# Kernel tuning notes

Hardware: AMD Instinct MI355X
Metric: run time of the kernel (lower is better)

The kernel has to match this reference:

```python
import jax, jax.numpy as jnp
import numpy as np

N = 50000   # nodes
E = 800000  # edges
IN, HID, OUT, H = 128, 256, 128, 4
C1 = HID // H  # per-head channels for conv1/conv2
EPS_LN = 1e-5


def layer_norm(x, g, b):
    mu = x.mean(-1, keepdims=True)
    var = ((x - mu) ** 2).mean(-1, keepdims=True)
    return (x - mu) * jax.lax.rsqrt(var + EPS_LN) * g + b


def gatv2(x, src, dst, edge_attr, Wl, bl, Wr, br, We, att, bias, heads, ch, n):
    # PyG GATv2Conv (concat=True, negative_slope=0.2, share_weights=False)
    xl = (x @ Wl + bl).reshape(-1, heads, ch)   # [N,H,C] source transform
    xr = (x @ Wr + br).reshape(-1, heads, ch)   # [N,H,C] target transform
    e = (edge_attr @ We).reshape(-1, heads, ch) # [E,H,C] edge transform (no bias)
    m = jax.nn.leaky_relu(xl[src] + xr[dst] + e, 0.2)     # [E,H,C]
    logits = jnp.einsum('ehc,hc->eh', m, att)             # [E,H]
    mx = jax.ops.segment_max(logits, dst, num_segments=n) # segment softmax over dst
    a = jnp.exp(logits - mx[dst])
    denom = jax.ops.segment_sum(a, dst, num_segments=n)
    alpha = a / (denom[dst] + 1e-16)                      # [E,H]
    out = jax.ops.segment_sum(xl[src] * alpha[..., None], dst, num_segments=n)
    return out.reshape(-1, heads * ch) + bias


def setup_inputs() -> dict:
    key = jax.random.key(0)
    ks = jax.random.split(key, 24)
    s = 0.05
    inp = {
        'x': jax.random.normal(ks[0], (N, IN), jnp.float32),
        'edge_index': jax.random.randint(ks[1], (2, E), 0, N, jnp.int32),
        'edge_attr': jax.random.uniform(ks[2], (E, 1), jnp.float32),
        # conv1: in=IN, out per head=C1, heads=H
        'Wl1': jax.random.normal(ks[3], (IN, HID)) * s,  'bl1': jnp.zeros((HID,)),
        'Wr1': jax.random.normal(ks[4], (IN, HID)) * s,  'br1': jnp.zeros((HID,)),
        'We1': jax.random.normal(ks[5], (1, HID)) * s,
        'att1': jax.random.normal(ks[6], (H, C1)) * s,   'bo1': jnp.zeros((HID,)),
        'g1': jnp.ones((HID,)), 'be1': jnp.zeros((HID,)),
        # conv2: in=HID
        'Wl2': jax.random.normal(ks[7], (HID, HID)) * s, 'bl2': jnp.zeros((HID,)),
        'Wr2': jax.random.normal(ks[8], (HID, HID)) * s, 'br2': jnp.zeros((HID,)),
        'We2': jax.random.normal(ks[9], (1, HID)) * s,
        'att2': jax.random.normal(ks[10], (H, C1)) * s,  'bo2': jnp.zeros((HID,)),
        'g2': jnp.ones((HID,)), 'be2': jnp.zeros((HID,)),
        # conv3: heads=1, out=OUT
        'Wl3': jax.random.normal(ks[11], (HID, OUT)) * s, 'bl3': jnp.zeros((OUT,)),
        'Wr3': jax.random.normal(ks[12], (HID, OUT)) * s, 'br3': jnp.zeros((OUT,)),
        'We3': jax.random.normal(ks[13], (1, OUT)) * s,
        'att3': jax.random.normal(ks[14], (1, OUT)) * s,  'bo3': jnp.zeros((OUT,)),
        'g3': jnp.ones((OUT,)), 'be3': jnp.zeros((OUT,)),
    }
    return inp


def reference(x, edge_index, edge_attr,
              Wl1, bl1, Wr1, br1, We1, att1, bo1, g1, be1,
              Wl2, bl2, Wr2, br2, We2, att2, bo2, g2, be2,
              Wl3, bl3, Wr3, br3, We3, att3, bo3, g3, be3):
    src, dst = edge_index[0], edge_index[1]
    h = gatv2(x, src, dst, edge_attr, Wl1, bl1, Wr1, br1, We1, att1, bo1, H, C1, N)
    h = jax.nn.elu(layer_norm(h, g1, be1))  # dropout inactive at inference
    h = gatv2(h, src, dst, edge_attr, Wl2, bl2, Wr2, br2, We2, att2, bo2, H, C1, N)
    h = jax.nn.elu(layer_norm(h, g2, be2))
    h = gatv2(h, src, dst, edge_attr, Wl3, bl3, Wr3, br3, We3, att3, bo3, 1, OUT, N)
    return layer_norm(h, g3, be3)
```

## Files before the change

kernel.cpp:

```cpp
#include <hip/hip_runtime.h>
#include <cstdint>
#include <cstddef>

typedef unsigned short u16;
typedef __attribute__((ext_vector_type(8))) short short8v;
typedef __attribute__((ext_vector_type(4))) float f32x4;

#define IN_DIM 128
#define HID_DIM 256
#define OUT_DIM 128
#define HEADS 4

__device__ __forceinline__ float b2f(u16 v) {
    return __uint_as_float(((unsigned)v) << 16);
}
__device__ __forceinline__ u16 f2b(float f) {
    unsigned u = __float_as_uint(f);
    u += 0x7fffu + ((u >> 16) & 1u);
    return (u16)(u >> 16);
}


__global__ void count_k(const int* __restrict__ dst, int* __restrict__ counts, int ne) {
    int i = blockIdx.x * blockDim.x + threadIdx.x;
    if (i < ne) atomicAdd(&counts[dst[i]], 1);
}

__global__ __launch_bounds__(1024) void scan_k(const int* __restrict__ counts,
                                               int* __restrict__ offs,
                                               int* __restrict__ cursor, int n) {
    __shared__ int wtot[16];
    __shared__ int carry_s;
    int tid = threadIdx.x, wv = tid >> 6, ln = tid & 63;
    if (tid == 0) carry_s = 0;
    __syncthreads();
    for (int base = 0; base < n; base += 4096) {
        int i0 = base + tid * 4;
        int4 c4 = {0, 0, 0, 0};
        if (i0 + 3 < n) c4 = *(const int4*)(counts + i0);
        else {
            if (i0     < n) c4.x = counts[i0];
            if (i0 + 1 < n) c4.y = counts[i0 + 1];
            if (i0 + 2 < n) c4.z = counts[i0 + 2];
            if (i0 + 3 < n) c4.w = counts[i0 + 3];
        }
        int s0 = c4.x, s1 = s0 + c4.y, s2 = s1 + c4.z, s3 = s2 + c4.w;
        int v = s3;
#pragma unroll
        for (int o = 1; o < 64; o <<= 1) {
            int t = __shfl_up(v, o);
            if (ln >= o) v += t;
        }
        if (ln == 63) wtot[wv] = v;
        int wpref = v - s3;
        __syncthreads();
        if (wv == 0) {
            int w2 = (ln < 16) ? wtot[ln] : 0;
#pragma unroll
            for (int o = 1; o < 16; o <<= 1) {
                int t = __shfl_up(w2, o);
                if (ln >= o) w2 += t;
            }
            if (ln < 16) wtot[ln] = w2;
        }
        __syncthreads();
        int wbase = carry_s + (wv ? wtot[wv - 1] : 0);
        int ex0 = wbase + wpref;
        if (i0     < n) { offs[i0]     = ex0;      cursor[i0]     = ex0; }
        if (i0 + 1 < n) { offs[i0 + 1] = ex0 + s0; cursor[i0 + 1] = ex0 + s0; }
        if (i0 + 2 < n) { offs[i0 + 2] = ex0 + s1; cursor[i0 + 2] = ex0 + s1; }
        if (i0 + 3 < n) { offs[i0 + 3] = ex0 + s2; cursor[i0 + 3] = ex0 + s2; }
        __syncthreads();
        if (tid == 0) carry_s += wtot[15];
        __syncthreads();
    }
    if (threadIdx.x == 0) offs[n] = carry_s;
}

__global__ void fill_k(const int* __restrict__ src, const int* __restrict__ dst,
                       const float* __restrict__ ea, int* __restrict__ cursor,
                       int* __restrict__ csrc, float* __restrict__ cea, int ne) {
    int i = blockIdx.x * blockDim.x + threadIdx.x;
    if (i < ne) {
        int p = atomicAdd(&cursor[dst[i]], 1);
        csrc[p] = src[i];
        cea[p] = ea[i];
    }
}


template <int KG>
__global__ void xpack_k(const float* __restrict__ X, short* __restrict__ Xp, int total) {
    int gid = blockIdx.x * blockDim.x + threadIdx.x;
    if (gid >= total) return;
    int lane = gid & 63;
    int kg = (gid >> 6) % KG;
    int rt = gid / (64 * KG);
    int row = rt * 16 + (lane & 15);
    int k0 = kg * 32 + ((lane >> 4) << 3);
    const float* src = X + (size_t)row * (KG * 32) + k0;
    short8v o;
#pragma unroll
    for (int j = 0; j < 8; j++) o[j] = (short)f2b(src[j]);
    ((short8v*)Xp)[gid] = o;
}

template <int K, int HOUT>
__global__ void packw_k(const float* __restrict__ Wl, const float* __restrict__ Wr,
                        short* __restrict__ Wp) {
    constexpr int KG = K / 32;
    int gid = blockIdx.x * blockDim.x + threadIdx.x;
    int lane = gid & 63;
    int kg = (gid >> 6) % KG;
    int nt = gid / (64 * KG);
    int col = nt * 16 + (lane & 15);
    int k0 = kg * 32 + ((lane >> 4) << 3);
    const float* Wsrc = (col < HOUT) ? Wl : Wr;
    int c2 = (col < HOUT) ? col : col - HOUT;
    short8v o;
#pragma unroll
    for (int j = 0; j < 8; j++) o[j] = (short)f2b(Wsrc[(size_t)(k0 + j) * HOUT + c2]);
    ((short8v*)Wp)[gid] = o;
}


template <int KG, int NT, int HOUT, int R>
__global__ __launch_bounds__(256) void gemm_mfma(
    const short* __restrict__ Xp, const short* __restrict__ Wp,
    const float* __restrict__ bl, const float* __restrict__ br,
    u16* __restrict__ XL, u16* __restrict__ XR, int nrt) {
    constexpr int NCG = NT / 8;
    int w = threadIdx.x >> 6, lane = threadIdx.x & 63;
    int cg = blockIdx.x % NCG;
    int rt0 = (blockIdx.x / NCG) * R;
    if (rt0 >= nrt) return;
    int rcnt = min(R, nrt - rt0);
    int nt0 = cg * 8 + w * 2;
    const short8v* wb = (const short8v*)Wp + lane;
    short8v wf0[KG], wf1[KG];
#pragma unroll
    for (int kg = 0; kg < KG; kg++) {
        wf0[kg] = wb[(size_t)(nt0 * KG + kg) * 64];
        wf1[kg] = wb[(size_t)((nt0 + 1) * KG + kg) * 64];
    }
    int colg0 = nt0 * 16 + ((lane >> 4) << 2);
    int colg1 = colg0 + 16;
    bool isr0 = colg0 >= HOUT;
    bool isr1 = colg1 >= HOUT;
    int cl0 = colg0 - (isr0 ? HOUT : 0);
    int cl1 = colg1 - (isr1 ? HOUT : 0);
    float4 bb0 = *(const float4*)((isr0 ? br : bl) + cl0);
    float4 bb1 = *(const float4*)((isr1 ? br : bl) + cl1);
    u16* ob0 = (isr0 ? XR : XL) + cl0;
    u16* ob1 = (isr1 ? XR : XL) + cl1;

    const short8v* xb = (const short8v*)Xp + (size_t)rt0 * KG * 64 + lane;
    for (int r = 0; r < rcnt; ++r) {
        f32x4 acc0 = {0.f, 0.f, 0.f, 0.f}, acc1 = {0.f, 0.f, 0.f, 0.f};
#pragma unroll
        for (int kg = 0; kg < KG; kg++) {
            short8v xf = xb[(size_t)(r * KG + kg) * 64];
            acc0 = __builtin_amdgcn_mfma_f32_16x16x32_bf16(wf0[kg], xf, acc0, 0, 0, 0);
            acc1 = __builtin_amdgcn_mfma_f32_16x16x32_bf16(wf1[kg], xf, acc1, 0, 0, 0);
        }
        size_t rowoff = (size_t)((rt0 + r) * 16 + (lane & 15)) * HOUT;
        ushort4 o0 = { f2b(acc0[0] + bb0.x), f2b(acc0[1] + bb0.y),
                       f2b(acc0[2] + bb0.z), f2b(acc0[3] + bb0.w) };
        *(ushort4*)(ob0 + rowoff) = o0;
        ushort4 o1 = { f2b(acc1[0] + bb1.x), f2b(acc1[1] + bb1.y),
                       f2b(acc1[2] + bb1.z), f2b(acc1[3] + bb1.w) };
        *(ushort4*)(ob1 + rowoff) = o1;
    }
}


__global__ __launch_bounds__(256) void gat_fused4(
    const int* __restrict__ offs, const int* __restrict__ csrc, const float* __restrict__ cea,
    const float* __restrict__ We, const float* __restrict__ att,
    const u16* __restrict__ XL, const u16* __restrict__ XR,
    const float* __restrict__ bo, const float* __restrict__ g, const float* __restrict__ be,
    u16* __restrict__ hp, int n) {
    __shared__ int   sS[4][64];
    __shared__ float sEA[4][64];
    int tid = threadIdx.x;
    int w = tid >> 6;
    int lane = tid & 63;
    int node = blockIdx.x * 4 + w;
    int es = lane >> 5;
    int ls = lane & 31;
    int cabs = ls * 8;
    float xr[8], wev[8], atv[8];
    {
        short8v x8 = *(const short8v*)(XR + (size_t)node * 256 + cabs);
        float4 wA = *(const float4*)(We + cabs), wB = *(const float4*)(We + cabs + 4);
        float4 aA = *(const float4*)(att + cabs), aB = *(const float4*)(att + cabs + 4);
#pragma unroll
        for (int i = 0; i < 8; i++) xr[i] = b2f((u16)x8[i]);
        wev[0] = wA.x; wev[1] = wA.y; wev[2] = wA.z; wev[3] = wA.w;
        wev[4] = wB.x; wev[5] = wB.y; wev[6] = wB.z; wev[7] = wB.w;
        atv[0] = aA.x; atv[1] = aA.y; atv[2] = aA.z; atv[3] = aA.w;
        atv[4] = aB.x; atv[5] = aB.y; atv[6] = aB.z; atv[7] = aB.w;
    }
    int b0 = offs[node], eEnd = offs[node + 1];
    float dsum = 0.f;
    float acc[8];
#pragma unroll
    for (int i = 0; i < 8; i++) acc[i] = 0.f;
    for (int base = b0; base < eEnd; base += 64) {
        int cnt = min(64, eEnd - base);
        if (lane < cnt) { sS[w][lane] = csrc[base + lane]; sEA[w][lane] = cea[base + lane]; }
        short8v r0, r1, r2;
        float e0, e1f, e2;
        bool v0, v1, v2;
        {
            int j0 = es, j1 = es + 2, j2 = es + 4;
            v0 = j0 < cnt; v1 = j1 < cnt; v2 = j2 < cnt;
            int i0 = v0 ? j0 : 0, i1 = v1 ? j1 : 0, i2 = v2 ? j2 : 0;
            e0 = sEA[w][i0]; r0 = *(const short8v*)(XL + (size_t)sS[w][i0] * 256 + cabs);
            e1f = sEA[w][i1]; r1 = *(const short8v*)(XL + (size_t)sS[w][i1] * 256 + cabs);
            e2 = sEA[w][i2]; r2 = *(const short8v*)(XL + (size_t)sS[w][i2] * 256 + cabs);
        }
        for (int r = 0; r < cnt; r += 2) {
            short8v rc = r0; float ec = e0; bool vc = v0;
            r0 = r1; e0 = e1f; v0 = v1;
            r1 = r2; e1f = e2; v1 = v2;
            int jn = r + 6 + es;
            v2 = jn < cnt;
            int idx = v2 ? jn : 0;
            e2 = sEA[w][idx];
            r2 = *(const short8v*)(XL + (size_t)sS[w][idx] * 256 + cabs);
            float x[8];
#pragma unroll
            for (int i = 0; i < 8; i++) x[i] = b2f((u16)rc[i]);
            float p = 0.f;
#pragma unroll
            for (int i = 0; i < 8; i++) {
                float t = fmaf(ec, wev[i], x[i]) + xr[i];
                t = fmaxf(t, 0.2f * t);
                p += t * atv[i];
            }
            p += __shfl_xor(p, 1);
            p += __shfl_xor(p, 2);
            p += __shfl_xor(p, 4);
            float wv2 = vc ? __expf(p) : 0.f;
            dsum += wv2;
#pragma unroll
            for (int i = 0; i < 8; i++) acc[i] += wv2 * x[i];
        }
    }
    dsum += __shfl_xor(dsum, 32);
#pragma unroll
    for (int i = 0; i < 8; i++) acc[i] += __shfl_xor(acc[i], 32);
    float inv = 1.f / (dsum + 1e-16f);
    float4 bA = *(const float4*)(bo + cabs), bB = *(const float4*)(bo + cabs + 4);
    float v[8];
    v[0] = acc[0] * inv + bA.x; v[1] = acc[1] * inv + bA.y;
    v[2] = acc[2] * inv + bA.z; v[3] = acc[3] * inv + bA.w;
    v[4] = acc[4] * inv + bB.x; v[5] = acc[5] * inv + bB.y;
    v[6] = acc[6] * inv + bB.z; v[7] = acc[7] * inv + bB.w;
    float s1 = 0.f, s2 = 0.f;
#pragma unroll
    for (int i = 0; i < 8; i++) { s1 += v[i]; s2 += v[i] * v[i]; }
#pragma unroll
    for (int o = 16; o >= 1; o >>= 1) {
        s1 += __shfl_xor(s1, o);
        s2 += __shfl_xor(s2, o);
    }
    float mu = s1 / 256.f;
    float sinv = rsqrtf(s2 / 256.f - mu * mu + 1e-5f);
    if (es == 0) {
        float4 gA = *(const float4*)(g + cabs), gB = *(const float4*)(g + cabs + 4);
        float4 eA = *(const float4*)(be + cabs), eB = *(const float4*)(be + cabs + 4);
        float gg[8] = {gA.x, gA.y, gA.z, gA.w, gB.x, gB.y, gB.z, gB.w};
        float ee[8] = {eA.x, eA.y, eA.z, eA.w, eB.x, eB.y, eB.z, eB.w};
        short8v yv;
#pragma unroll
        for (int i = 0; i < 8; i++) {
            float y = (v[i] - mu) * sinv * gg[i] + ee[i];
            y = (y > 0.f) ? y : expm1f(y);
            yv[i] = (short)f2b(y);
        }
        int kg = cabs >> 5;
        int l = (node & 15) | (((cabs >> 3) & 3) << 4);
        size_t eoff = (((size_t)(node >> 4) * 8 + kg) * 64 + l) * 8;
        *(short8v*)(hp + eoff) = yv;
    }
}


__global__ __launch_bounds__(256) void gat_fused1(
    const int* __restrict__ offs, const int* __restrict__ csrc, const float* __restrict__ cea,
    const float* __restrict__ We, const float* __restrict__ att,
    const u16* __restrict__ XL, const u16* __restrict__ XR,
    const float* __restrict__ bo, const float* __restrict__ g, const float* __restrict__ be,
    float* __restrict__ out, int n) {
    __shared__ int   sS[4][64];
    __shared__ float sEA[4][64];
    int tid = threadIdx.x;
    int w = tid >> 6;
    int lane = tid & 63;
    int node = blockIdx.x * 4 + w;
    int q = lane >> 4;
    int ls = lane & 15;
    int cb = ls * 8;
    float xr[8], wev[8], atv[8];
    {
        short8v x8 = *(const short8v*)(XR + (size_t)node * 128 + cb);
        float4 wA = *(const float4*)(We + cb), wB = *(const float4*)(We + cb + 4);
        float4 aA = *(const float4*)(att + cb), aB = *(const float4*)(att + cb + 4);
#pragma unroll
        for (int i = 0; i < 8; i++) xr[i] = b2f((u16)x8[i]);
        wev[0] = wA.x; wev[1] = wA.y; wev[2] = wA.z; wev[3] = wA.w;
        wev[4] = wB.x; wev[5] = wB.y; wev[6] = wB.z; wev[7] = wB.w;
        atv[0] = aA.x; atv[1] = aA.y; atv[2] = aA.z; atv[3] = aA.w;
        atv[4] = aB.x; atv[5] = aB.y; atv[6] = aB.z; atv[7] = aB.w;
    }
    int b0 = offs[node], eEnd = offs[node + 1];
    float dsum = 0.f;
    float acc[8];
#pragma unroll
    for (int i = 0; i < 8; i++) acc[i] = 0.f;
    for (int base = b0; base < eEnd; base += 64) {
        int cnt = min(64, eEnd - base);
        if (lane < cnt) { sS[w][lane] = csrc[base + lane]; sEA[w][lane] = cea[base + lane]; }
        short8v r0, r1, r2;
        float e0, e1f, e2;
        bool v0, v1, v2;
        {
            int j0 = q, j1 = q + 4, j2 = q + 8;
            v0 = j0 < cnt; v1 = j1 < cnt; v2 = j2 < cnt;
            int i0 = v0 ? j0 : 0, i1 = v1 ? j1 : 0, i2 = v2 ? j2 : 0;
            e0 = sEA[w][i0]; r0 = *(const short8v*)(XL + (size_t)sS[w][i0] * 128 + cb);
            e1f = sEA[w][i1]; r1 = *(const short8v*)(XL + (size_t)sS[w][i1] * 128 + cb);
            e2 = sEA[w][i2]; r2 = *(const short8v*)(XL + (size_t)sS[w][i2] * 128 + cb);
        }
        for (int r = 0; r < cnt; r += 4) {
            short8v rc = r0; float ec = e0; bool vc = v0;
            r0 = r1; e0 = e1f; v0 = v1;
            r1 = r2; e1f = e2; v1 = v2;
            int jn = r + 12 + q;
            v2 = jn < cnt;
            int idx = v2 ? jn : 0;
            e2 = sEA[w][idx];
            r2 = *(const short8v*)(XL + (size_t)sS[w][idx] * 128 + cb);
            float x[8];
#pragma unroll
            for (int i = 0; i < 8; i++) x[i] = b2f((u16)rc[i]);
            float p = 0.f;
#pragma unroll
            for (int i = 0; i < 8; i++) {
                float t = fmaf(ec, wev[i], x[i]) + xr[i];
                t = fmaxf(t, 0.2f * t);
                p += t * atv[i];
            }
            p += __shfl_xor(p, 1);
            p += __shfl_xor(p, 2);
            p += __shfl_xor(p, 4);
            p += __shfl_xor(p, 8);
            float wv2 = vc ? __expf(p) : 0.f;
            dsum += wv2;
#pragma unroll
            for (int i = 0; i < 8; i++) acc[i] += wv2 * x[i];
        }
    }
    dsum += __shfl_xor(dsum, 32);
    dsum += __shfl_xor(dsum, 16);
#pragma unroll
    for (int i = 0; i < 8; i++) {
        acc[i] += __shfl_xor(acc[i], 32);
        acc[i] += __shfl_xor(acc[i], 16);
    }
    float inv = 1.f / (dsum + 1e-16f);
    float4 bA = *(const float4*)(bo + cb), bB = *(const float4*)(bo + cb + 4);
    float v[8];
    v[0] = acc[0] * inv + bA.x; v[1] = acc[1] * inv + bA.y;
    v[2] = acc[2] * inv + bA.z; v[3] = acc[3] * inv + bA.w;
    v[4] = acc[4] * inv + bB.x; v[5] = acc[5] * inv + bB.y;
    v[6] = acc[6] * inv + bB.z; v[7] = acc[7] * inv + bB.w;
    float s1 = 0.f, s2 = 0.f;
#pragma unroll
    for (int i = 0; i < 8; i++) { s1 += v[i]; s2 += v[i] * v[i]; }
#pragma unroll
    for (int o = 8; o >= 1; o >>= 1) {
        s1 += __shfl_xor(s1, o);
        s2 += __shfl_xor(s2, o);
    }
    float mu = s1 / 128.f;
    float sinv = rsqrtf(s2 / 128.f - mu * mu + 1e-5f);
    if (q == 0) {
        float4 gA = *(const float4*)(g + cb), gB = *(const float4*)(g + cb + 4);
        float4 eA = *(const float4*)(be + cb), eB = *(const float4*)(be + cb + 4);
        float gg[8] = {gA.x, gA.y, gA.z, gA.w, gB.x, gB.y, gB.z, gB.w};
        float ee[8] = {eA.x, eA.y, eA.z, eA.w, eB.x, eB.y, eB.z, eB.w};
        float4 oA, oB;
        oA.x = (v[0] - mu) * sinv * gg[0] + ee[0];
        oA.y = (v[1] - mu) * sinv * gg[1] + ee[1];
        oA.z = (v[2] - mu) * sinv * gg[2] + ee[2];
        oA.w = (v[3] - mu) * sinv * gg[3] + ee[3];
        oB.x = (v[4] - mu) * sinv * gg[4] + ee[4];
        oB.y = (v[5] - mu) * sinv * gg[5] + ee[5];
        oB.z = (v[6] - mu) * sinv * gg[6] + ee[6];
        oB.w = (v[7] - mu) * sinv * gg[7] + ee[7];
        float* op = out + (size_t)node * 128 + cb;
        *(float4*)op = oA;
        *(float4*)(op + 4) = oB;
    }
}


extern "C" void kernel_launch(void* const* d_in, const int* in_sizes, int n_in,
                              void* d_out, int out_size, void* d_ws, size_t ws_size,
                              hipStream_t stream) {
    const float* x  = (const float*)d_in[0];
    const int*   ei = (const int*)d_in[1];
    const float* ea = (const float*)d_in[2];
    const float *Wl1 = (const float*)d_in[3],  *bl1 = (const float*)d_in[4];
    const float *Wr1 = (const float*)d_in[5],  *br1 = (const float*)d_in[6];
    const float *We1 = (const float*)d_in[7],  *att1 = (const float*)d_in[8];
    const float *bo1 = (const float*)d_in[9],  *g1 = (const float*)d_in[10], *be1 = (const float*)d_in[11];
    const float *Wl2 = (const float*)d_in[12], *bl2 = (const float*)d_in[13];
    const float *Wr2 = (const float*)d_in[14], *br2 = (const float*)d_in[15];
    const float *We2 = (const float*)d_in[16], *att2 = (const float*)d_in[17];
    const float *bo2 = (const float*)d_in[18], *g2 = (const float*)d_in[19], *be2 = (const float*)d_in[20];
    const float *Wl3 = (const float*)d_in[21], *bl3 = (const float*)d_in[22];
    const float *Wr3 = (const float*)d_in[23], *br3 = (const float*)d_in[24];
    const float *We3 = (const float*)d_in[25], *att3 = (const float*)d_in[26];
    const float *bo3 = (const float*)d_in[27], *g3 = (const float*)d_in[28], *be3 = (const float*)d_in[29];

    int n = in_sizes[0] / IN_DIM;
    int e = in_sizes[1] / 2;
    const int* srcv = ei;
    const int* dstv = ei + e;
    int nrt = n / 16;

    char* w = (char*)d_ws;
    size_t off = 0;
    auto take = [&](size_t bytes) -> void* {
        void* p = w + off;
        off = (off + bytes + 255) & ~(size_t)255;
        return p;
    };
    int*   counts = (int*)take((size_t)n * 4);
    int*   cursor = (int*)take((size_t)n * 4);
    int*   offs   = (int*)take((size_t)(n + 1) * 4);
    int*   csrc   = (int*)take((size_t)e * 4);
    float* ceaw   = (float*)take((size_t)e * 4);
    u16*   XL     = (u16*)take((size_t)n * HID_DIM * 2);
    u16*   XR     = (u16*)take((size_t)n * HID_DIM * 2);
    short* xpack  = (short*)take((size_t)nrt * 4 * 64 * 8 * 2);
    short* hpack  = (short*)take((size_t)nrt * 8 * 64 * 8 * 2);
    short* wp1    = (short*)take((size_t)32 * 4 * 64 * 8 * 2);
    short* wp2    = (short*)take((size_t)32 * 8 * 64 * 8 * 2);
    short* wp3    = (short*)take((size_t)16 * 8 * 64 * 8 * 2);

    const int TPB = 256;
    int eb = (e + TPB - 1) / TPB;

    hipMemsetAsync(counts, 0, (size_t)n * 4, stream);
    count_k<<<eb, TPB, 0, stream>>>(dstv, counts, e);
    scan_k<<<1, 1024, 0, stream>>>(counts, offs, cursor, n);
    fill_k<<<eb, TPB, 0, stream>>>(srcv, dstv, ea, cursor, csrc, ceaw, e);

    packw_k<IN_DIM,  HID_DIM><<<32 * 4 * 64 / TPB, TPB, 0, stream>>>(Wl1, Wr1, wp1);
    packw_k<HID_DIM, HID_DIM><<<32 * 8 * 64 / TPB, TPB, 0, stream>>>(Wl2, Wr2, wp2);
    packw_k<HID_DIM, OUT_DIM><<<16 * 8 * 64 / TPB, TPB, 0, stream>>>(Wl3, Wr3, wp3);
    int xtot = nrt * 4 * 64;
    xpack_k<4><<<(xtot + TPB - 1) / TPB, TPB, 0, stream>>>(x, xpack, xtot);

    gemm_mfma<4, 32, HID_DIM, 8><<<4 * ((nrt + 7) / 8), TPB, 0, stream>>>(
        xpack, wp1, bl1, br1, XL, XR, nrt);
    gat_fused4<<<n / 4, 256, 0, stream>>>(
        offs, csrc, ceaw, We1, att1, XL, XR, bo1, g1, be1, (u16*)hpack, n);

    gemm_mfma<8, 32, HID_DIM, 8><<<4 * ((nrt + 7) / 8), TPB, 0, stream>>>(
        hpack, wp2, bl2, br2, XL, XR, nrt);
    gat_fused4<<<n / 4, 256, 0, stream>>>(
        offs, csrc, ceaw, We2, att2, XL, XR, bo2, g2, be2, (u16*)hpack, n);

    gemm_mfma<8, 16, OUT_DIM, 4><<<2 * ((nrt + 3) / 4), TPB, 0, stream>>>(
        hpack, wp3, bl3, br3, XL, XR, nrt);
    gat_fused1<<<n / 4, 256, 0, stream>>>(
        offs, csrc, ceaw, We3, att3, XL, XR, bo3, g3, be3, (float*)d_out, n);
}
```

Baseline: 441.9 us.

## Schedule GAT aggregation nodes in descending in-degree order via counting-sort permutation

Builds a permutation of nodes sorted by in-degree, descending, using a histogram, scan and scatter over degree buckets. The three fused GAT aggregation kernels then take their node index from this permutation, so the four wavefronts in a block handle nodes of similar degree and heavy nodes start first. The aim is to cut intra-block imbalance and tail effects from the variable degree. It adds three small kernels plus a memset, and breaks the sequential node order, which may reduce locality of XR and output accesses.

```diff
diff --git a/kernel.cpp b/kernel.cpp
--- a/kernel.cpp
+++ b/kernel.cpp
@@ -89,6 +89,37 @@
 }
 
 
+__global__ void dhist_k(const int* __restrict__ counts, int* __restrict__ dh, int n) {
+    int i = blockIdx.x * blockDim.x + threadIdx.x;
+    if (i < n) atomicAdd(&dh[127 - min(counts[i], 127)], 1);
+}
+
+__global__ __launch_bounds__(128) void dscan_k(int* __restrict__ dh) {
+    __shared__ int s[128];
+    int t = threadIdx.x;
+    int own = dh[t];
+    s[t] = own;
+    __syncthreads();
+    for (int o = 1; o < 128; o <<= 1) {
+        int v = (t >= o) ? s[t - o] : 0;
+        __syncthreads();
+        s[t] += v;
+        __syncthreads();
+    }
+    dh[t] = s[t] - own;
+}
+
+__global__ void dscatter_k(const int* __restrict__ counts, int* __restrict__ dh,
+                           int* __restrict__ perm, int n) {
+    int i = blockIdx.x * blockDim.x + threadIdx.x;
+    if (i < n) {
+        int b = 127 - min(counts[i], 127);
+        int p = atomicAdd(&dh[b], 1);
+        perm[p] = i;
+    }
+}
+
+
 template <int KG>
 __global__ void xpack_k(const float* __restrict__ X, short* __restrict__ Xp, int total) {
     int gid = blockIdx.x * blockDim.x + threadIdx.x;
@@ -175,6 +206,7 @@
 
 
 __global__ __launch_bounds__(256) void gat_fused4(
+    const int* __restrict__ perm,
     const int* __restrict__ offs, const int* __restrict__ csrc, const float* __restrict__ cea,
     const float* __restrict__ We, const float* __restrict__ att,
     const u16* __restrict__ XL, const u16* __restrict__ XR,
@@ -185,7 +217,7 @@
     int tid = threadIdx.x;
     int w = tid >> 6;
     int lane = tid & 63;
-    int node = blockIdx.x * 4 + w;
+    int node = perm[blockIdx.x * 4 + w];
     int es = lane >> 5;
     int ls = lane & 31;
     int cabs = ls * 8;
@@ -289,6 +321,7 @@
 
 
 __global__ __launch_bounds__(256) void gat_fused1(
+    const int* __restrict__ perm,
     const int* __restrict__ offs, const int* __restrict__ csrc, const float* __restrict__ cea,
     const float* __restrict__ We, const float* __restrict__ att,
     const u16* __restrict__ XL, const u16* __restrict__ XR,
@@ -299,7 +332,7 @@
     int tid = threadIdx.x;
     int w = tid >> 6;
     int lane = tid & 63;
-    int node = blockIdx.x * 4 + w;
+    int node = perm[blockIdx.x * 4 + w];
     int q = lane >> 4;
     int ls = lane & 15;
     int cb = ls * 8;
@@ -445,6 +478,8 @@
     int*   offs   = (int*)take((size_t)(n + 1) * 4);
     int*   csrc   = (int*)take((size_t)e * 4);
     float* ceaw   = (float*)take((size_t)e * 4);
+    int*   dh     = (int*)take(128 * 4);
+    int*   perm   = (int*)take((size_t)n * 4);
     u16*   XL     = (u16*)take((size_t)n * HID_DIM * 2);
     u16*   XR     = (u16*)take((size_t)n * HID_DIM * 2);
     short* xpack  = (short*)take((size_t)nrt * 4 * 64 * 8 * 2);
@@ -455,11 +490,17 @@
 
     const int TPB = 256;
     int eb = (e + TPB - 1) / TPB;
+    int nb = (n + TPB - 1) / TPB;
 
     hipMemsetAsync(counts, 0, (size_t)n * 4, stream);
+    hipMemsetAsync(dh, 0, 128 * 4, stream);
     count_k<<<eb, TPB, 0, stream>>>(dstv, counts, e);
     scan_k<<<1, 1024, 0, stream>>>(counts, offs, cursor, n);
     fill_k<<<eb, TPB, 0, stream>>>(srcv, dstv, ea, cursor, csrc, ceaw, e);
+
+    dhist_k<<<nb, TPB, 0, stream>>>(counts, dh, n);
+    dscan_k<<<1, 128, 0, stream>>>(dh);
+    dscatter_k<<<nb, TPB, 0, stream>>>(counts, dh, perm, n);
 
     packw_k<IN_DIM,  HID_DIM><<<32 * 4 * 64 / TPB, TPB, 0, stream>>>(Wl1, Wr1, wp1);
     packw_k<HID_DIM, HID_DIM><<<32 * 8 * 64 / TPB, TPB, 0, stream>>>(Wl2, Wr2, wp2);
@@ -470,15 +511,15 @@
     gemm_mfma<4, 32, HID_DIM, 8><<<4 * ((nrt + 7) / 8), TPB, 0, stream>>>(
         xpack, wp1, bl1, br1, XL, XR, nrt);
     gat_fused4<<<n / 4, 256, 0, stream>>>(
-        offs, csrc, ceaw, We1, att1, XL, XR, bo1, g1, be1, (u16*)hpack, n);
+        perm, offs, csrc, ceaw, We1, att1, XL, XR, bo1, g1, be1, (u16*)hpack, n);
 
     gemm_mfma<8, 32, HID_DIM, 8><<<4 * ((nrt + 7) / 8), TPB, 0, stream>>>(
         hpack, wp2, bl2, br2, XL, XR, nrt);
     gat_fused4<<<n / 4, 256, 0, stream>>>(
-        offs, csrc, ceaw, We2, att2, XL, XR, bo2, g2, be2, (u16*)hpack, n);
+        perm, offs, csrc, ceaw, We2, att2, XL, XR, bo2, g2, be2, (u16*)hpack, n);
 
     gemm_mfma<8, 16, OUT_DIM, 4><<<2 * ((nrt + 3) / 4), TPB, 0, stream>>>(
         hpack, wp3, bl3, br3, XL, XR, nrt);
     gat_fused1<<<n / 4, 256, 0, stream>>>(
-        offs, csrc, ceaw, We3, att3, XL, XR, bo3, g3, be3, (float*)d_out, n);
-}
+        perm, offs, csrc, ceaw, We3, att3, XL, XR, bo3, g3, be3, (float*)d_out, n);
+}
```

Result: slower. 731.1 us (+65.4%).
